# Kernel tuning notes

Hardware: AMD Instinct MI355X
Metric: run time of the kernel (lower is better)

## Reference

```python
import jax, jax.numpy as jnp
import numpy as np

L = 21          # number of kernel positions
C0, C1 = 32, 32 # kernel_channels
IN_DIM = 7      # 3 + 3 + 1 geometric features


def leaky_relu(x):
    return jnp.where(x >= 0, x, 0.2 * x)


def setup_inputs() -> dict:
    key = jax.random.key(0)
    k1, k2, k3, k4, k5 = jax.random.split(key, 5)
    E = 1_000_000
    inp = jax.random.normal(k1, (E, IN_DIM), dtype=jnp.float32)
    idx = jax.random.randint(k2, (E,), 0, L, dtype=jnp.int32)
    # kaiming-uniform style init for Ws, zeros for bs (per reset_parameters)
    def ku(k, shape):
        fan = shape[1] * shape[2]
        gain = np.sqrt(2.0 / (1 + np.sqrt(5) ** 2))
        bound = np.sqrt(3.0) * gain / np.sqrt(fan)
        return jax.random.uniform(k, shape, jnp.float32, -bound, bound)
    W0 = ku(k3, (L, IN_DIM, C0))
    b0 = jnp.zeros((L, C0), dtype=jnp.float32)
    W1 = ku(k4, (L, C0, C1))
    b1 = jnp.zeros((L, C1), dtype=jnp.float32)
    return {"input": inp, "idx": idx, "W0": W0, "b0": b0, "W1": W1, "b1": b1}


def reference(input, idx, W0, b0, W1, b1):
    # layer 0: gather per-edge [7, C0] weight, 1x7 @ 7xC0 matmul, bias, leaky-relu
    h = leaky_relu(jnp.einsum('ek,ekc->ec', input, W0[idx]) + b0[idx])
    # layer 1: gather per-edge [C0, C1] weight
    w = leaky_relu(jnp.einsum('ek,ekc->ec', h, W1[idx]) + b1[idx])
    return w
```

## Files before the change

kernel.cpp:

```cpp
#include <hip/hip_runtime.h>

#define L 21
#define C0 32
#define C1 32
#define IN_DIM 7
#define GHIST 256
#define BPAD 256

__global__ __launch_bounds__(256) void k_hist(const int* __restrict__ idx, int E,
                                              int* __restrict__ blockCounts) {
  __shared__ int h[L];
  int tid = threadIdx.x;
  if (tid < L) h[tid] = 0;
  __syncthreads();
  int per = (E + GHIST - 1) / GHIST;
  int s = blockIdx.x * per;
  int e = min(E, s + per);
  for (int i = s + tid; i < e; i += blockDim.x)
    atomicAdd(&h[idx[i]], 1);
  __syncthreads();
  if (tid < L) blockCounts[blockIdx.x * L + tid] = h[tid];
}

__global__ __launch_bounds__(256) void k_scan(const int* __restrict__ blockCounts,
                                              int* __restrict__ cursor,
                                              int* __restrict__ endArr,
                                              int* __restrict__ blockL,
                                              int nBlk) {
  __shared__ int tot[L];
  __shared__ int base[L + 1];
  int tid = threadIdx.x;
  if (tid < L) {
    int s = 0;
#pragma unroll 8
    for (int b = 0; b < GHIST; b++) s += blockCounts[b * L + tid];
    tot[tid] = s;
  }
  __syncthreads();
  if (tid == 0) {
    int a = 0;
    for (int l = 0; l < L; l++) { base[l] = a; a += (tot[l] + BPAD - 1) & ~(BPAD - 1); }
    base[L] = a;
  }
  __syncthreads();
  if (tid < L) {
    int a = base[tid];
#pragma unroll 8
    for (int b = 0; b < GHIST; b++) {
      cursor[b * L + tid] = a;
      a += blockCounts[b * L + tid];
    }
    endArr[tid] = base[tid] + tot[tid];
  }
  __syncthreads();
  for (int blk = tid; blk < nBlk; blk += 256) {
    int pos = blk * 256;
    int lv = -1;
#pragma unroll
    for (int l = 0; l < L; l++)
      if (pos >= base[l] && pos < base[l + 1]) lv = l;
    blockL[blk] = lv;
  }
}

__global__ __launch_bounds__(256) void k_scatter(const int* __restrict__ idx,
                                                 const float* __restrict__ inp, int E,
                                                 const int* __restrict__ cursor,
                                                 int* __restrict__ perm,
                                                 float* __restrict__ xb) {
  __shared__ int cur[L];
  int tid = threadIdx.x;
  if (tid < L) cur[tid] = cursor[blockIdx.x * L + tid];
  __syncthreads();
  int per = (E + GHIST - 1) / GHIST;
  int s = blockIdx.x * per;
  int e = min(E, s + per);
  for (int i = s + tid; i < e; i += blockDim.x) {
    int l = idx[i];
    int pos = atomicAdd(&cur[l], 1);
    perm[pos] = i;
    const float* row = inp + (size_t)i * IN_DIM;
    float4 a, b;
    a.x = row[0]; a.y = row[1]; a.z = row[2]; a.w = row[3];
    b.x = row[4]; b.y = row[5]; b.z = row[6]; b.w = 0.f;
    float4* dst = (float4*)(xb + (size_t)pos * 8);
    dst[0] = a;
    dst[1] = b;
  }
}

template <bool USE_XB>
__global__ __launch_bounds__(256) void k_compute(const float* __restrict__ xb,
                                                 const float* __restrict__ inp,
                                                 const float* __restrict__ W0g,
                                                 const float* __restrict__ b0g,
                                                 const float* __restrict__ W1g,
                                                 const float* __restrict__ b1g,
                                                 const int* __restrict__ perm,
                                                 const int* __restrict__ blockL,
                                                 const int* __restrict__ endArr,
                                                 float* __restrict__ out) {
  int l = blockL[blockIdx.x];
  if (l < 0) return;
  l = __builtin_amdgcn_readfirstlane(l);
  int end = __builtin_amdgcn_readfirstlane(endArr[l]);

  int T = threadIdx.x;
  int blockbase = blockIdx.x * 256;
  int slot = blockbase + T;

  float x[IN_DIM];
  if (USE_XB) {
    const float4* xrow = (const float4*)(xb + (size_t)slot * 8);
    float4 xa = xrow[0], xc = xrow[1];
    x[0] = xa.x; x[1] = xa.y; x[2] = xa.z; x[3] = xa.w;
    x[4] = xc.x; x[5] = xc.y; x[6] = xc.z;
  } else {
    int p0 = slot < end ? perm[slot] : 0;
    const float* row = inp + (size_t)p0 * IN_DIM;
#pragma unroll
    for (int k = 0; k < IN_DIM; k++) x[k] = row[k];
  }

  const float* w0 = W0g + l * (IN_DIM * C0);
  const float* B0 = b0g + l * C0;
  const float* w1 = W1g + l * (C0 * C1);
  const float* B1 = b1g + l * C1;

  float h[C0];
#pragma unroll
  for (int c = 0; c < C0; c++) h[c] = B0[c];
#pragma unroll
  for (int k = 0; k < IN_DIM; k++) {
#pragma unroll
    for (int c = 0; c < C0; c++) h[c] = fmaf(x[k], w0[k * C0 + c], h[c]);
  }
#pragma unroll
  for (int c = 0; c < C0; c++) h[c] = h[c] >= 0.f ? h[c] : 0.2f * h[c];

  float o[C1];
#pragma unroll
  for (int c = 0; c < C1; c++) o[c] = B1[c];
#pragma unroll
  for (int k = 0; k < C0; k++) {
#pragma unroll
    for (int c = 0; c < C1; c++) o[c] = fmaf(h[k], w1[k * C1 + c], o[c]);
  }
#pragma unroll
  for (int c = 0; c < C1; c++) o[c] = o[c] >= 0.f ? o[c] : 0.2f * o[c];

  __shared__ float obuf[256 * 32];
#pragma unroll
  for (int cq = 0; cq < 32; cq += 4) {
    int ad = T * 32 + (cq ^ ((T & 7) << 2));
    float4 v = {o[cq], o[cq + 1], o[cq + 2], o[cq + 3]};
    *(float4*)&obuf[ad] = v;
  }
  __syncthreads();
  int cq = (T & 7) * 4;
#pragma unroll
  for (int j = 0; j < 8; j++) {
    int r = j * 32 + (T >> 3);
    int slot_r = blockbase + r;
    if (slot_r < end) {
      int p = perm[slot_r];
      float4 v = *(const float4*)&obuf[r * 32 + (cq ^ ((r & 7) << 2))];
      *(float4*)(out + (size_t)p * C1 + cq) = v;
    }
  }
}

extern "C" void kernel_launch(void* const* d_in, const int* in_sizes, int n_in,
                              void* d_out, int out_size, void* d_ws, size_t ws_size,
                              hipStream_t stream) {
  const float* inp = (const float*)d_in[0];
  const int* idx   = (const int*)d_in[1];
  const float* W0  = (const float*)d_in[2];
  const float* b0  = (const float*)d_in[3];
  const float* W1  = (const float*)d_in[4];
  const float* b1  = (const float*)d_in[5];
  float* out = (float*)d_out;
  int E = in_sizes[1];

  int nBlk = (E + 255) / 256 + L;
  size_t slots = (size_t)nBlk * 256;

  int* ws = (int*)d_ws;
  int* blockCounts = ws;
  int* cursor      = blockCounts + GHIST * L;
  int* endArr      = cursor + GHIST * L;
  int* blockL      = endArr + L;
  int* perm        = blockL + nBlk;
  size_t ints = (size_t)2 * GHIST * L + L + nBlk + slots;
  ints = (ints + 3) & ~(size_t)3;
  float* xb = (float*)(ws + ints);
  size_t need = ints * 4 + slots * 8 * 4;
  bool use_xb = ws_size >= need;

  k_hist<<<GHIST, 256, 0, stream>>>(idx, E, blockCounts);
  k_scan<<<1, 256, 0, stream>>>(blockCounts, cursor, endArr, blockL, nBlk);

  if (use_xb) {
    k_scatter<<<GHIST, 256, 0, stream>>>(idx, inp, E, cursor, perm, xb);
    k_compute<true><<<nBlk, 256, 0, stream>>>(xb, inp, W0, b0, W1, b1,
                                              perm, blockL, endArr, out);
  } else {
    k_scatter<<<GHIST, 256, 0, stream>>>(idx, inp, E, cursor, perm, xb);
    k_compute<false><<<nBlk, 256, 0, stream>>>(nullptr, inp, W0, b0, W1, b1,
                                               perm, blockL, endArr, out);
  }
}
```

Before: 94.01 us.

## Compute block level via ballot over bases and shrink output staging LDS

Removes the per-block level table from the single-block scan kernel. Each compute block now derives its level by ballot and popcount over the padded base offsets. The output staging buffer shrinks from 32 KB to 8 KB by staging one wavefront at a time over four rounds with extra barriers. This is meant to raise occupancy and shorten the serial scan, at the cost of more synchronisation in the epilogue.

```diff
diff --git a/kernel.cpp b/kernel.cpp
--- a/kernel.cpp
+++ b/kernel.cpp
@@ -25,8 +25,7 @@
 __global__ __launch_bounds__(256) void k_scan(const int* __restrict__ blockCounts,
                                               int* __restrict__ cursor,
                                               int* __restrict__ endArr,
-                                              int* __restrict__ blockL,
-                                              int nBlk) {
+                                              int* __restrict__ baseArr) {
   __shared__ int tot[L];
   __shared__ int base[L + 1];
   int tid = threadIdx.x;
@@ -52,15 +51,7 @@
     }
     endArr[tid] = base[tid] + tot[tid];
   }
-  __syncthreads();
-  for (int blk = tid; blk < nBlk; blk += 256) {
-    int pos = blk * 256;
-    int lv = -1;
-#pragma unroll
-    for (int l = 0; l < L; l++)
-      if (pos >= base[l] && pos < base[l + 1]) lv = l;
-    blockL[blk] = lv;
-  }
+  if (tid <= L) baseArr[tid] = base[tid];
 }
 
 __global__ __launch_bounds__(256) void k_scatter(const int* __restrict__ idx,
@@ -97,16 +88,20 @@
                                                  const float* __restrict__ W1g,
                                                  const float* __restrict__ b1g,
                                                  const int* __restrict__ perm,
-                                                 const int* __restrict__ blockL,
+                                                 const int* __restrict__ baseArr,
                                                  const int* __restrict__ endArr,
                                                  float* __restrict__ out) {
-  int l = blockL[blockIdx.x];
-  if (l < 0) return;
+  int T = threadIdx.x;
+  int lane = T & 63;
+  int blockbase = blockIdx.x << 8;
+
+  int bv = baseArr[lane <= L ? lane : L];
+  unsigned long long m = __ballot((lane <= L) && (blockbase >= bv));
+  int l = __popcll(m) - 1;
+  if (l >= L) return;
   l = __builtin_amdgcn_readfirstlane(l);
   int end = __builtin_amdgcn_readfirstlane(endArr[l]);
 
-  int T = threadIdx.x;
-  int blockbase = blockIdx.x * 256;
   int slot = blockbase + T;
 
   float x[IN_DIM];
@@ -149,24 +144,32 @@
 #pragma unroll
   for (int c = 0; c < C1; c++) o[c] = o[c] >= 0.f ? o[c] : 0.2f * o[c];
 
-  __shared__ float obuf[256 * 32];
-#pragma unroll
-  for (int cq = 0; cq < 32; cq += 4) {
-    int ad = T * 32 + (cq ^ ((T & 7) << 2));
-    float4 v = {o[cq], o[cq + 1], o[cq + 2], o[cq + 3]};
-    *(float4*)&obuf[ad] = v;
-  }
-  __syncthreads();
-  int cq = (T & 7) * 4;
-#pragma unroll
-  for (int j = 0; j < 8; j++) {
-    int r = j * 32 + (T >> 3);
-    int slot_r = blockbase + r;
+  __shared__ float obuf[64 * 32];
+  int wv = T >> 6;
+  int row = T >> 2;
+  int q = (T & 3) * 8;
+#pragma unroll
+  for (int c = 0; c < 4; c++) {
+    if (wv == c) {
+#pragma unroll
+      for (int cq = 0; cq < 32; cq += 4) {
+        int ad = lane * 32 + (cq ^ ((lane & 7) << 2));
+        float4 v = {o[cq], o[cq + 1], o[cq + 2], o[cq + 3]};
+        *(float4*)&obuf[ad] = v;
+      }
+    }
+    __syncthreads();
+    int slot_r = blockbase + c * 64 + row;
     if (slot_r < end) {
       int p = perm[slot_r];
-      float4 v = *(const float4*)&obuf[r * 32 + (cq ^ ((r & 7) << 2))];
-      *(float4*)(out + (size_t)p * C1 + cq) = v;
+      int sw = (row & 7) << 2;
+      float4 v0 = *(const float4*)&obuf[row * 32 + (q ^ sw)];
+      float4 v1 = *(const float4*)&obuf[row * 32 + ((q + 4) ^ sw)];
+      float* dst = out + (size_t)p * C1 + q;
+      *(float4*)dst = v0;
+      *(float4*)(dst + 4) = v1;
     }
+    if (c < 3) __syncthreads();
   }
 }
 
@@ -189,24 +192,23 @@
   int* blockCounts = ws;
   int* cursor      = blockCounts + GHIST * L;
   int* endArr      = cursor + GHIST * L;
-  int* blockL      = endArr + L;
-  int* perm        = blockL + nBlk;
-  size_t ints = (size_t)2 * GHIST * L + L + nBlk + slots;
+  int* baseArr     = endArr + L;
+  int* perm        = baseArr + (L + 1);
+  size_t ints = (size_t)2 * GHIST * L + L + (L + 1) + slots;
   ints = (ints + 3) & ~(size_t)3;
   float* xb = (float*)(ws + ints);
   size_t need = ints * 4 + slots * 8 * 4;
   bool use_xb = ws_size >= need;
 
   k_hist<<<GHIST, 256, 0, stream>>>(idx, E, blockCounts);
-  k_scan<<<1, 256, 0, stream>>>(blockCounts, cursor, endArr, blockL, nBlk);
+  k_scan<<<1, 256, 0, stream>>>(blockCounts, cursor, endArr, baseArr);
+  k_scatter<<<GHIST, 256, 0, stream>>>(idx, inp, E, cursor, perm, xb);
 
   if (use_xb) {
-    k_scatter<<<GHIST, 256, 0, stream>>>(idx, inp, E, cursor, perm, xb);
     k_compute<true><<<nBlk, 256, 0, stream>>>(xb, inp, W0, b0, W1, b1,
-                                              perm, blockL, endArr, out);
+                                              perm, baseArr, endArr, out);
   } else {
-    k_scatter<<<GHIST, 256, 0, stream>>>(idx, inp, E, cursor, perm, xb);
     k_compute<false><<<nBlk, 256, 0, stream>>>(nullptr, inp, W0, b0, W1, b1,
-                                               perm, blockL, endArr, out);
-  }
-}
+                                               perm, baseArr, endArr, out);
+  }
+}
```

Result: faster. 89.54 us (-4.8%).
